# Kernel optimization log

Hardware: AMD Instinct MI355X
Metric: run time of the kernel (lower is better)

## Reference

```python
import jax, jax.numpy as jnp
import numpy as np

B, P, K = 32, 1024, 20  # clouds, points per cloud, kNN neighbors
EPS = 1e-5


def knn_idx(x, k):
    # x: [B,P,d] -> indices of k nearest neighbors (squared L2, includes self), [B,P,k]
    d2 = jnp.sum(x * x, axis=-1)
    dist = d2[:, :, None] + d2[:, None, :] - 2.0 * jnp.einsum('bpd,bqd->bpq', x, x)
    _, idx = jax.lax.top_k(-dist, k)
    return idx


def edge_conv(x, idx, msg_fn):
    # gather neighbor features, build [x_i, x_j - x_i] edge features, max-aggregate
    xj = jax.vmap(lambda xb, ib: xb[ib])(x, idx)            # [B,P,K,d]
    xi = jnp.broadcast_to(x[:, :, None, :], xj.shape)       # [B,P,K,d]
    e = jnp.concatenate([xi, xj - xi], axis=-1)             # [B,P,K,2d]
    return jnp.max(msg_fn(e), axis=2)                       # [B,P,out]


def setup_inputs() -> dict:
    key = jax.random.key(0)
    ks = jax.random.split(key, 5)
    s = 0.05
    return {
        'pos': jax.random.normal(ks[0], (B * P, 3), jnp.float32),
        'W1a': jax.random.normal(ks[1], (6, 64), jnp.float32) * s,
        'b1a': jnp.zeros((64,), jnp.float32),
        'g1': jnp.ones((64,), jnp.float32),
        'be1': jnp.zeros((64,), jnp.float32),
        'W1b': jax.random.normal(ks[2], (64, 64), jnp.float32) * s,
        'b1b': jnp.zeros((64,), jnp.float32),
        'W2': jax.random.normal(ks[3], (128, 128), jnp.float32) * s,
        'b2': jnp.zeros((128,), jnp.float32),
        'Wl': jax.random.normal(ks[4], (192, 128), jnp.float32) * s,
        'bl': jnp.zeros((128,), jnp.float32),
        'batch': jnp.repeat(jnp.arange(B, dtype=jnp.int32), P),
    }


def reference(pos, W1a, b1a, g1, be1, W1b, b1b, W2, b2, Wl, bl, batch):
    # batch is uniform-sized and sorted -> fixed reshape to [B,P,.]
    x0 = pos.reshape(B, P, 3)

    def mlp1(e):  # Linear(6,64) -> BatchNorm -> ReLU -> Linear(64,64)
        h = e @ W1a + b1a
        mu = jnp.mean(h, axis=(0, 1, 2))
        var = jnp.var(h, axis=(0, 1, 2))
        h = (h - mu) * jax.lax.rsqrt(var + EPS) * g1 + be1
        h = jax.nn.relu(h)
        return h @ W1b + b1b

    x1 = edge_conv(x0, knn_idx(x0, K), mlp1)                         # [B,P,64]
    x2 = edge_conv(x1, knn_idx(x1, K), lambda e: e @ W2 + b2)        # [B,P,128]
    h = jnp.concatenate([x1, x2], axis=-1) @ Wl + bl                 # [B,P,128]
    return jnp.max(h, axis=1)                                        # global_max_pool -> [B,128]
```

## Files before the change

### kernel.cpp

```cpp
#include <hip/hip_runtime.h>
#include <cfloat>
#include <cstdint>

#define NB 32
#define NP 1024
#define NK 20
#define NPTS 32768

typedef __attribute__((ext_vector_type(8))) short bf16x8;
typedef __attribute__((ext_vector_type(4))) float f32x4;

__device__ __forceinline__ unsigned bf16rne(float v) {
  const unsigned u = __float_as_uint(v);
  return (u + 0x7fffu + ((u >> 16) & 1u)) >> 16;
}

__device__ __forceinline__ float unsort_f(unsigned s) {
  const unsigned m = (~(unsigned)((int)s >> 31)) | 0x80000000u;
  return __uint_as_float(s ^ m);
}

__global__ __launch_bounds__(256) void kd2(const float* __restrict__ x, int dim,
                                           float* __restrict__ d2) {
  int p = blockIdx.x * 256 + threadIdx.x;
  if (p >= NPTS) return;
  if (dim == 64) {
    const float4* xr = (const float4*)(x + (size_t)p * 64);
    float s = 0.f;
#pragma unroll
    for (int dq = 0; dq < 16; dq++) {
      float4 v = xr[dq];
      s = fmaf(v.x, v.x, s);
      s = fmaf(v.y, v.y, s);
      s = fmaf(v.z, v.z, s);
      s = fmaf(v.w, v.w, s);
    }
    d2[p] = s;
  } else {
    float s = 0.f;
#pragma unroll
    for (int d = 0; d < 3; d++) {
      float v = x[p * 3 + d];
      s = fmaf(v, v, s);
    }
    d2[p] = s;
  }
}

__global__ __launch_bounds__(256) void kxprep(const float* __restrict__ x,
                                              unsigned short* __restrict__ Xh,
                                              unsigned short* __restrict__ Xl) {
  const int t = blockIdx.x * 256 + threadIdx.x;
  const int p = t >> 3, g = t & 7;
  const float4* xr = (const float4*)(x + (size_t)p * 64 + g * 8);
  const float4 v0 = xr[0];
  const float4 v1 = xr[1];
  const float vv[8] = {v0.x, v0.y, v0.z, v0.w, v1.x, v1.y, v1.z, v1.w};
  unsigned short h[8], l[8];
#pragma unroll
  for (int j = 0; j < 8; j++) {
    const float z = vv[j];
    const unsigned u = __float_as_uint(z);
    const unsigned hb = (u + 0x7fffu + ((u >> 16) & 1u)) & 0xffff0000u;
    h[j] = (unsigned short)(hb >> 16);
    l[j] = (unsigned short)bf16rne(z - __uint_as_float(hb));
  }
  const int off = (((p >> 4) * 2 + (g >> 2)) * 64 + ((g & 3) << 4) + (p & 15)) * 8;
  *(uint4*)&Xh[off] = *(const uint4*)&h[0];
  *(uint4*)&Xl[off] = *(const uint4*)&l[0];
}

__global__ __launch_bounds__(256) void kdistm(const unsigned short* __restrict__ Xh,
                                              const unsigned short* __restrict__ Xl,
                                              const float* __restrict__ d2,
                                              int c0, int nc, float* __restrict__ D) {
  const int lane = threadIdx.x & 63;
  const int w = threadIdx.x >> 6;
  const int cloud = blockIdx.x % nc;
  const int t = blockIdx.x / nc;
  const int tr0 = (t >> 3) * 128, tc0 = (t & 7) * 128;
  const int cb = (c0 + cloud) * 1024;
  const int rw = tr0 + w * 32;

  bf16x8 Ah[2][2], Al[2][2];
#pragma unroll
  for (int mt = 0; mt < 2; mt++)
#pragma unroll
    for (int ks = 0; ks < 2; ks++) {
      const int tg = (cb + rw + mt * 16) >> 4;
      const size_t base = ((size_t)(tg * 2 + ks) * 64 + lane) * 8;
      Ah[mt][ks] = *(const bf16x8*)&Xh[base];
      Al[mt][ks] = *(const bf16x8*)&Xl[base];
    }
  float d2r[2][4];
#pragma unroll
  for (int mt = 0; mt < 2; mt++)
#pragma unroll
    for (int r = 0; r < 4; r++)
      d2r[mt][r] = d2[cb + rw + mt * 16 + (lane >> 4) * 4 + r];

  for (int nt = 0; nt < 8; nt++) {
    const int cg = cb + tc0 + nt * 16;
    bf16x8 Bh2[2], Bl2[2];
#pragma unroll
    for (int ks = 0; ks < 2; ks++) {
      const int tg = cg >> 4;
      const size_t base = ((size_t)(tg * 2 + ks) * 64 + lane) * 8;
      Bh2[ks] = *(const bf16x8*)&Xh[base];
      Bl2[ks] = *(const bf16x8*)&Xl[base];
    }
    const float d2c = d2[cg + (lane & 15)];
#pragma unroll
    for (int mt = 0; mt < 2; mt++) {
      f32x4 C = {0.f, 0.f, 0.f, 0.f};
      C = __builtin_amdgcn_mfma_f32_16x16x32_bf16(Ah[mt][0], Bh2[0], C, 0, 0, 0);
      C = __builtin_amdgcn_mfma_f32_16x16x32_bf16(Ah[mt][0], Bl2[0], C, 0, 0, 0);
      C = __builtin_amdgcn_mfma_f32_16x16x32_bf16(Al[mt][0], Bh2[0], C, 0, 0, 0);
      C = __builtin_amdgcn_mfma_f32_16x16x32_bf16(Ah[mt][1], Bh2[1], C, 0, 0, 0);
      C = __builtin_amdgcn_mfma_f32_16x16x32_bf16(Ah[mt][1], Bl2[1], C, 0, 0, 0);
      C = __builtin_amdgcn_mfma_f32_16x16x32_bf16(Al[mt][1], Bh2[1], C, 0, 0, 0);
#pragma unroll
      for (int r = 0; r < 4; r++) {
        const int row = cloud * 1024 + rw + mt * 16 + (lane >> 4) * 4 + r;
        const int col = tc0 + nt * 16 + (lane & 15);
        D[(size_t)row * 1024 + col] = fmaf(-2.f, C[r], d2r[mt][r] + d2c);
      }
    }
  }
}

__device__ __forceinline__ void select20(const float* dv, unsigned long long* w,
                                         int lane, int pg, int gbase,
                                         int* __restrict__ idxo) {
  unsigned k32[16];
#pragma unroll
  for (int ii = 0; ii < 16; ii++) {
    unsigned u = __float_as_uint(dv[ii]);
    u ^= (((int)u >> 31) | 0x80000000u);
    k32[ii] = u;
  }
  unsigned lmn = k32[0];
#pragma unroll
  for (int ii = 1; ii < 16; ii++) lmn = k32[ii] < lmn ? k32[ii] : lmn;
  unsigned mn = lmn, mlm = lmn;
#pragma unroll
  for (int s = 1; s < 64; s <<= 1) {
    const unsigned a = __shfl_xor(mn, s, 64);
    const unsigned b = __shfl_xor(mlm, s, 64);
    mn = a < mn ? a : mn;
    mlm = b > mlm ? b : mlm;
  }
  unsigned lo32 = mn;
  unsigned long long hi32 = (unsigned long long)mlm + 1;
  float flo = unsort_f(mn), fhi = unsort_f(mlm);
  float clo = 0.f, chi = 140.f;
  unsigned m32 = 0;
  bool found = false;
  for (int it = 0; it < 40; ++it) {
    if (hi32 - (unsigned long long)lo32 <= 1) break;
    unsigned m;
    if (it < 6) {
      float fr = (42.f - clo) / (chi - clo);
      fr = fr < 0.04f ? 0.04f : (fr > 0.96f ? 0.96f : fr);
      const float pf = fmaf(fhi - flo, fr, flo);
      unsigned u = __float_as_uint(pf);
      u ^= (((int)u >> 31) | 0x80000000u);
      m = u;
      if (m <= lo32) m = lo32 + 1;
      if ((unsigned long long)m >= hi32) m = (unsigned)(hi32 - 1);
    } else {
      m = (unsigned)(lo32 + ((hi32 - lo32) >> 1));
    }
    int cnt = 0;
#pragma unroll
    for (int ii = 0; ii < 16; ii++) cnt += __popcll(__ballot(k32[ii] < m));
    if (cnt < 20) {
      lo32 = m;
      flo = unsort_f(m);
      clo = (float)cnt;
    } else if (cnt > 64) {
      hi32 = m;
      fhi = unsort_f(m);
      chi = (float)cnt;
    } else {
      m32 = m;
      found = true;
      break;
    }
  }

  if (found) {
    unsigned mask = 0;
#pragma unroll
    for (int ii = 0; ii < 16; ii++) mask |= (k32[ii] < m32) ? (1u << ii) : 0u;
    const int lc = __popc(mask);
    int x = lc;
#pragma unroll
    for (int s = 1; s < 64; s <<= 1) {
      const int y = __shfl_up(x, s, 64);
      if (lane >= s) x += y;
    }
    int off = x - lc;
    w[lane] = ~0ULL;
    __builtin_amdgcn_wave_barrier();
#pragma unroll
    for (int i = 0; i < 4; i++)
#pragma unroll
      for (int j = 0; j < 4; j++) {
        const int ii = i * 4 + j;
        if ((mask & (1u << ii)) && off < 64) {
          w[off] = ((unsigned long long)k32[ii] << 10) |
                   (unsigned)(i * 256 + (lane << 2) + j);
          off++;
        }
      }
    __builtin_amdgcn_wave_barrier();
    unsigned long long K = w[lane];
#pragma unroll
    for (int k = 2; k <= 64; k <<= 1) {
#pragma unroll
      for (int j2 = k >> 1; j2 > 0; j2 >>= 1) {
        const unsigned long long o = __shfl_xor(K, j2, 64);
        const bool takeMin = (((lane & j2) == 0) == ((lane & k) == 0));
        const bool lt = K < o;
        const unsigned long long sml = lt ? K : o;
        const unsigned long long big = lt ? o : K;
        K = takeMin ? sml : big;
      }
    }
    if (lane < NK) idxo[(size_t)pg * NK + lane] = gbase + (int)(K & 1023u);
  } else {
    unsigned long long lo64 = ((unsigned long long)lo32) << 10;
    unsigned long long hi64 = hi32 << 10;
    unsigned long long cut = hi64;
    for (int it = 0; it < 48 && (hi64 - lo64) > 1; ++it) {
      const unsigned long long m = lo64 + ((hi64 - lo64) >> 1);
      int cnt = 0;
#pragma unroll
      for (int ii = 0; ii < 16; ii++) {
        const unsigned long long key =
            ((unsigned long long)k32[ii] << 10) |
            (unsigned)(((ii >> 2) << 8) + (lane << 2) + (ii & 3));
        cnt += __popcll(__ballot(key < m));
      }
      if (cnt == 20) {
        cut = m;
        break;
      }
      if (cnt < 20)
        lo64 = m;
      else
        hi64 = m;
      cut = hi64;
    }
    int base = 0;
#pragma unroll
    for (int ii = 0; ii < 16; ii++) {
      const unsigned long long key =
          ((unsigned long long)k32[ii] << 10) |
          (unsigned)(((ii >> 2) << 8) + (lane << 2) + (ii & 3));
      const unsigned long long b = __ballot(key < cut);
      if (key < cut) {
        const int slot = base + __builtin_amdgcn_mbcnt_hi(
                                    (unsigned)(b >> 32),
                                    __builtin_amdgcn_mbcnt_lo((unsigned)b, 0));
        idxo[(size_t)pg * NK + slot] = gbase + (int)(key & 1023u);
      }
      base += __popcll(b);
    }
  }
}

__global__ __launch_bounds__(512) void kfsel1(const float* __restrict__ pos,
                                              const float* __restrict__ d2,
                                              int* __restrict__ idxo) {
  __shared__ float px[1024], py[1024], pz[1024], pd2[1024];
  __shared__ unsigned long long lw[8][64];
  const int tid = threadIdx.x;
  const int lane = tid & 63;
  const int w = tid >> 6;
  const int cloud = blockIdx.x >> 7;
  const int mb = blockIdx.x & 127;
  const int cb = cloud << 10;

  if (tid < 256) {
    const float4* ppos = (const float4*)(pos + (size_t)cb * 3 + tid * 12);
    const float4 a = ppos[0], b = ppos[1], c = ppos[2];
    *(float4*)&px[tid * 4] = make_float4(a.x, a.w, b.z, c.y);
    *(float4*)&py[tid * 4] = make_float4(a.y, b.x, b.w, c.z);
    *(float4*)&pz[tid * 4] = make_float4(a.z, b.y, c.x, c.w);
  }
  *(float2*)&pd2[tid * 2] = *(const float2*)(d2 + cb + tid * 2);
  __syncthreads();

  const int pl = mb * 8 + w;
  const float xi0 = px[pl], xi1 = py[pl], xi2 = pz[pl];
  const float dp = pd2[pl];
  float dv[16];
#pragma unroll
  for (int i = 0; i < 4; i++) {
    const float4 X = *(const float4*)&px[i * 256 + lane * 4];
    const float4 Y = *(const float4*)&py[i * 256 + lane * 4];
    const float4 Z = *(const float4*)&pz[i * 256 + lane * 4];
    const float4 Q = *(const float4*)&pd2[i * 256 + lane * 4];
    const float xs[4] = {X.x, X.y, X.z, X.w};
    const float ys[4] = {Y.x, Y.y, Y.z, Y.w};
    const float zs[4] = {Z.x, Z.y, Z.z, Z.w};
    const float qs[4] = {Q.x, Q.y, Q.z, Q.w};
#pragma unroll
    for (int j = 0; j < 4; j++) {
      float acc = 0.f;
      acc = fmaf(xi0, xs[j], acc);
      acc = fmaf(xi1, ys[j], acc);
      acc = fmaf(xi2, zs[j], acc);
      dv[i * 4 + j] = fmaf(-2.f, acc, dp + qs[j]);
    }
  }
  select20(dv, lw[w], lane, cb + pl, cb, idxo);
}

__global__ __launch_bounds__(256) void kselect2(const float* __restrict__ D,
                                                int c0, int* __restrict__ idxo) {
  __shared__ unsigned long long lw[4][64];
  const int lane = threadIdx.x & 63;
  const int sub = threadIdx.x >> 6;
  const int pchunk = blockIdx.x * 4 + sub;
  const int pg = c0 * 1024 + pchunk;
  const int gbase = (pg >> 10) << 10;

  float dv[16];
  const float4* dr = (const float4*)(D + (size_t)pchunk * 1024 + lane * 4);
#pragma unroll
  for (int i = 0; i < 4; i++) {
    const float4 d4 = dr[i * 64];
    dv[i * 4 + 0] = d4.x;
    dv[i * 4 + 1] = d4.y;
    dv[i * 4 + 2] = d4.z;
    dv[i * 4 + 3] = d4.w;
  }
  select20(dv, lw[sub], lane, pg, gbase, idxo);
}

__global__ __launch_bounds__(256) void kstats(const float* __restrict__ pos,
                                              const int* __restrict__ idx,
                                              double* __restrict__ Spart) {
  __shared__ float red[4][42];
  const int tid = threadIdx.x;
  const int w = tid >> 6;
  int p = blockIdx.x * 256 + tid;
  float xi0 = pos[p * 3], xi1 = pos[p * 3 + 1], xi2 = pos[p * 3 + 2];
  float s1[6];
  float s2[36];
#pragma unroll
  for (int a = 0; a < 6; a++) s1[a] = 0.f;
#pragma unroll
  for (int a = 0; a < 36; a++) s2[a] = 0.f;
  for (int k = 0; k < NK; k++) {
    int j = idx[p * NK + k];
    float e[6];
    e[0] = xi0;
    e[1] = xi1;
    e[2] = xi2;
    e[3] = pos[j * 3] - xi0;
    e[4] = pos[j * 3 + 1] - xi1;
    e[5] = pos[j * 3 + 2] - xi2;
#pragma unroll
    for (int a = 0; a < 6; a++) {
      s1[a] += e[a];
#pragma unroll
      for (int b = 0; b < 6; b++) s2[a * 6 + b] = fmaf(e[a], e[b], s2[a * 6 + b]);
    }
  }
#pragma unroll
  for (int a = 0; a < 6; a++) {
#pragma unroll
    for (int m = 1; m < 64; m <<= 1) s1[a] += __shfl_xor(s1[a], m, 64);
  }
#pragma unroll
  for (int a = 0; a < 36; a++) {
#pragma unroll
    for (int m = 1; m < 64; m <<= 1) s2[a] += __shfl_xor(s2[a], m, 64);
  }
  if ((tid & 63) == 0) {
#pragma unroll
    for (int a = 0; a < 6; a++) red[w][a] = s1[a];
#pragma unroll
    for (int a = 0; a < 36; a++) red[w][6 + a] = s2[a];
  }
  __syncthreads();
  if (tid < 42) {
    double t = (double)red[0][tid] + (double)red[1][tid] + (double)red[2][tid] +
               (double)red[3][tid];
    Spart[(size_t)blockIdx.x * 42 + tid] = t;
  }
}

__global__ void kbn(const double* __restrict__ Spart, const float* __restrict__ W1a,
                    const float* __restrict__ b1a, const float* __restrict__ g1,
                    const float* __restrict__ be1, const float* __restrict__ W1b,
                    float* __restrict__ ss, unsigned short* __restrict__ Bh,
                    unsigned short* __restrict__ Bl) {
  __shared__ double S[42];
  const int c = threadIdx.x;
  if (c < 42) {
    double t = 0.0;
    for (int b = 0; b < 128; b++) t += Spart[(size_t)b * 42 + c];
    S[c] = t;
  }
  for (int t = c; t < 4096; t += 256) {
    const int j = t & 7, L = (t >> 3) & 63, f = t >> 9;
    const int nt = f >> 1, ks = f & 1;
    const int k = ks * 32 + (L >> 4) * 8 + j;
    const int n = nt * 16 + (L & 15);
    const float wv = W1b[k * 64 + n];
    const unsigned u = __float_as_uint(wv);
    const unsigned hb = (u + 0x7fffu + ((u >> 16) & 1u)) & 0xffff0000u;
    Bh[t] = (unsigned short)(hb >> 16);
    Bl[t] = (unsigned short)bf16rne(wv - __uint_as_float(hb));
  }
  __syncthreads();
  if (c < 64) {
    double w[6];
#pragma unroll
    for (int d = 0; d < 6; d++) w[d] = (double)W1a[d * 64 + c];
    double b = (double)b1a[c];
    const double invN = 1.0 / (double)((size_t)NPTS * NK);
    double m1 = 0.0;
#pragma unroll
    for (int d = 0; d < 6; d++) m1 += w[d] * S[d];
    m1 *= invN;
    double q = 0.0;
#pragma unroll
    for (int a = 0; a < 6; a++)
#pragma unroll
      for (int d = 0; d < 6; d++) q += w[a] * w[d] * S[6 + a * 6 + d];
    q *= invN;
    double mu = m1 + b;
    double eh2 = q + 2.0 * b * m1 + b * b;
    double var = eh2 - mu * mu;
    if (var < 0.0) var = 0.0;
    double inv = 1.0 / sqrt(var + 1e-5);
    double sc = (double)g1[c] * inv;
    ss[c] = (float)sc;
    ss[64 + c] = (float)((double)be1[c] - mu * sc);
  }
}

#define EC1P 8
__global__ __launch_bounds__(256) void kec1(const float* __restrict__ pos,
                                            const int* __restrict__ idx,
                                            const float* __restrict__ ss,
                                            const float* __restrict__ W1a,
                                            const float* __restrict__ b1a,
                                            const unsigned short* __restrict__ Bh,
                                            const unsigned short* __restrict__ Bl,
                                            const float* __restrict__ b1b,
                                            float* __restrict__ x1) {
  __shared__ __align__(16) unsigned short Ah[4][3072];
  __shared__ __align__(16) unsigned short Al[4][3072];
  __shared__ float nbr[4][160];
  const int tid = threadIdx.x;
  const int lane = tid & 63;
  const int w = tid >> 6;
  const int p0 = blockIdx.x * EC1P + w * 2;

  unsigned short* ah = Ah[w];
  unsigned short* al = Al[w];
  float* nb = nbr[w];

  if (lane < 40) {
    const int j = idx[(size_t)p0 * NK + lane];
    nb[lane * 4 + 0] = pos[j * 3 + 0];
    nb[lane * 4 + 1] = pos[j * 3 + 1];
    nb[lane * 4 + 2] = pos[j * 3 + 2];
  }

  float wdf[3], wbt[3];
#pragma unroll
  for (int d = 0; d < 3; d++) {
    const float top = W1a[d * 64 + lane];
    const float bot = W1a[(3 + d) * 64 + lane];
    wdf[d] = top - bot;
    wbt[d] = bot;
  }
  const float b1 = b1a[lane];
  const float sc = ss[lane];
  const float sh = ss[64 + lane];
  const int lanehi = (((lane & 31) >> 3) * 128) + ((lane >> 5) * 512);
  const int lanelo = lane & 7;
  const int g3w = ((lane & 31) >> 3) + ((lane >> 5) << 2);
  __builtin_amdgcn_wave_barrier();

#pragma unroll
  for (int pp = 0; pp < 2; pp++) {
    const int p = p0 + pp;
    const float xi0 = pos[p * 3], xi1 = pos[p * 3 + 1], xi2 = pos[p * 3 + 2];
    const float pu = fmaf(xi2, wdf[2], fmaf(xi1, wdf[1], fmaf(xi0, wdf[0], b1)));
    for (int k = 0; k < NK; k++) {
      const int row = pp * NK + k;
      const float4 nbv = *(const float4*)&nb[row * 4];
      const float pv = fmaf(nbv.z, wbt[2], fmaf(nbv.y, wbt[1], nbv.x * wbt[0]));
      const float z = fmaxf(fmaf(pu + pv, sc, sh), 0.f);
      const unsigned u = __float_as_uint(z);
      const unsigned hb = (u + 0x7fffu + ((u >> 16) & 1u)) & 0xffff0000u;
      const int off =
          (row >> 4) * 1024 + lanehi + (((row & 15) ^ g3w) << 3) + lanelo;
      ah[off] = (unsigned short)(hb >> 16);
      al[off] = (unsigned short)bf16rne(z - __uint_as_float(hb));
    }
  }
  __builtin_amdgcn_wave_barrier();

  bf16x8 bh[4][2], bl[4][2];
#pragma unroll
  for (int nt = 0; nt < 4; nt++)
#pragma unroll
    for (int ks = 0; ks < 2; ks++) {
      const int base = ((nt * 2 + ks) * 64 + lane) * 8;
      bh[nt][ks] = *(const bf16x8*)&Bh[base];
      bl[nt][ks] = *(const bf16x8*)&Bl[base];
    }

  float pA[4], pB[4];
#pragma unroll
  for (int nt = 0; nt < 4; nt++) {
    pA[nt] = -FLT_MAX;
    pB[nt] = -FLT_MAX;
  }
  const int q4 = (lane >> 4) * 4;
  const int rb0 = (lane >> 4) * 128 + (((lane & 15) ^ (lane >> 4)) << 3);
  const int rb1 =
      512 + (lane >> 4) * 128 + (((lane & 15) ^ (4 + (lane >> 4))) << 3);

#pragma unroll
  for (int mt = 0; mt < 3; mt++) {
    const bf16x8 a_h0 = *(const bf16x8*)&ah[mt * 1024 + rb0];
    const bf16x8 a_l0 = *(const bf16x8*)&al[mt * 1024 + rb0];
    const bf16x8 a_h1 = *(const bf16x8*)&ah[mt * 1024 + rb1];
    const bf16x8 a_l1 = *(const bf16x8*)&al[mt * 1024 + rb1];
#pragma unroll
    for (int nt = 0; nt < 4; nt++) {
      f32x4 C = {0.f, 0.f, 0.f, 0.f};
      C = __builtin_amdgcn_mfma_f32_16x16x32_bf16(a_h0, bh[nt][0], C, 0, 0, 0);
      C = __builtin_amdgcn_mfma_f32_16x16x32_bf16(a_h0, bl[nt][0], C, 0, 0, 0);
      C = __builtin_amdgcn_mfma_f32_16x16x32_bf16(a_l0, bh[nt][0], C, 0, 0, 0);
      C = __builtin_amdgcn_mfma_f32_16x16x32_bf16(a_h1, bh[nt][1], C, 0, 0, 0);
      C = __builtin_amdgcn_mfma_f32_16x16x32_bf16(a_h1, bl[nt][1], C, 0, 0, 0);
      C = __builtin_amdgcn_mfma_f32_16x16x32_bf16(a_l1, bh[nt][1], C, 0, 0, 0);
#pragma unroll
      for (int r = 0; r < 4; r++) {
        const int row = mt * 16 + q4 + r;
        const float vv = C[r];
        if (row < NK) pA[nt] = fmaxf(pA[nt], vv);
        if (row >= NK && row < 2 * NK) pB[nt] = fmaxf(pB[nt], vv);
      }
    }
  }
#pragma unroll
  for (int s = 16; s < 64; s <<= 1) {
#pragma unroll
    for (int nt = 0; nt < 4; nt++) {
      pA[nt] = fmaxf(pA[nt], __shfl_xor(pA[nt], s, 64));
      pB[nt] = fmaxf(pB[nt], __shfl_xor(pB[nt], s, 64));
    }
  }
  if (lane < 16) {
#pragma unroll
    for (int nt = 0; nt < 4; nt++) {
      const float bb = b1b[nt * 16 + lane];
      x1[(size_t)p0 * 64 + nt * 16 + lane] = pA[nt] + bb;
      x1[(size_t)(p0 + 1) * 64 + nt * 16 + lane] = pB[nt] + bb;
    }
  }
}

__global__ __launch_bounds__(256) void kv(const float* __restrict__ x1,
                                          const float* __restrict__ W2,
                                          float* __restrict__ v) {
  const int c = threadIdx.x & 127;
  const int sub = threadIdx.x >> 7;
  float wv[64];
#pragma unroll
  for (int d = 0; d < 64; d++) wv[d] = W2[(64 + d) * 128 + c];
  const int pbase = blockIdx.x * 64 + sub * 32;
  for (int i = 0; i < 32; i++) {
    const int p = pbase + i;
    const float4* xr = (const float4*)(x1 + (size_t)p * 64);
    float a0 = 0.f, a1 = 0.f;
#pragma unroll
    for (int dq = 0; dq < 16; dq++) {
      float4 xv = xr[dq];
      a0 = fmaf(xv.x, wv[dq * 4 + 0], a0);
      a1 = fmaf(xv.y, wv[dq * 4 + 1], a1);
      a0 = fmaf(xv.z, wv[dq * 4 + 2], a0);
      a1 = fmaf(xv.w, wv[dq * 4 + 3], a1);
    }
    v[(size_t)p * 128 + c] = a0 + a1;
  }
}

__global__ __launch_bounds__(256) void kprep(const float* __restrict__ W2,
                                             const float* __restrict__ Wl,
                                             const float* __restrict__ b2,
                                             const float* __restrict__ bl,
                                             float* __restrict__ Bc,
                                             float* __restrict__ cb) {
  const int t = blockIdx.x * 256 + threadIdx.x;
  const int d = t >> 7, c = t & 127;
  float s = Wl[d * 128 + c];
  for (int e = 0; e < 128; e++)
    s = fmaf(W2[d * 128 + e] - W2[(64 + d) * 128 + e], Wl[(64 + e) * 128 + c], s);
  Bc[d * 128 + c] = s;
  Bc[(64 + 2 * d) * 128 + c] = Wl[(64 + 2 * d) * 128 + c];
  Bc[(64 + 2 * d + 1) * 128 + c] = Wl[(64 + 2 * d + 1) * 128 + c];
  if (d == 0) {
    float sb = bl[c];
    for (int e = 0; e < 128; e++) sb = fmaf(b2[e], Wl[(64 + e) * 128 + c], sb);
    cb[c] = sb;
  }
}

__global__ __launch_bounds__(256) void kprep2(const float* __restrict__ Bc,
                                              unsigned short* __restrict__ Bch,
                                              unsigned short* __restrict__ Bcl) {
  const int t = blockIdx.x * 256 + threadIdx.x;
  const int j = t & 7, L = (t >> 3) & 63, f = t >> 9;
  const int nt = f / 6, kc = f % 6;
  const int k = kc * 32 + ((L >> 4) << 3) + j;
  const int n = nt * 16 + (L & 15);
  const float wv = Bc[k * 128 + n];
  const unsigned u = __float_as_uint(wv);
  const unsigned hb = (u + 0x7fffu + ((u >> 16) & 1u)) & 0xffff0000u;
  Bch[t] = (unsigned short)(hb >> 16);
  Bcl[t] = (unsigned short)bf16rne(wv - __uint_as_float(hb));
}

__global__ __launch_bounds__(256) void kgemm(const float* __restrict__ x1,
                                             const float* __restrict__ v,
                                             const int* __restrict__ idx,
                                             const unsigned short* __restrict__ Bch,
                                             const unsigned short* __restrict__ Bcl,
                                             float* __restrict__ partial) {
  __shared__ int idxs[4][320];
  __shared__ __align__(16) float vlds[4][16][132];
  __shared__ float red[4][8][16];
  const int tid = threadIdx.x;
  const int lane = tid & 63;
  const int w = tid >> 6;
  const int cloud = blockIdx.x & 31;
  const int mb = blockIdx.x >> 5;
  const int pbase = cloud * 1024 + mb * 64;
  const int mrow = lane & 15, gsel = lane >> 4;
  const int m = w * 16 + mrow;

#pragma unroll
  for (int r = 0; r < 5; r++)
    idxs[w][r * 64 + lane] = idx[(size_t)(pbase + w * 16) * NK + r * 64 + lane];
  __builtin_amdgcn_wave_barrier();

  for (int pt = 0; pt < 16; pt++) {
    const int* ip = &idxs[w][pt * NK];
    float m0 = -FLT_MAX, m1 = -FLT_MAX;
#pragma unroll
    for (int k = 0; k < NK; k++) {
      const float2 val = *(const float2*)(v + (size_t)ip[k] * 128 + lane * 2);
      m0 = fmaxf(m0, val.x);
      m1 = fmaxf(m1, val.y);
    }
    *(float2*)&vlds[w][pt][lane * 2] = make_float2(m0, m1);
  }
  __builtin_amdgcn_wave_barrier();

  bf16x8 aH[6], aL[6];
#pragma unroll
  for (int kc = 0; kc < 2; kc++) {
    const float4* xr =
        (const float4*)(x1 + (size_t)(pbase + m) * 64 + kc * 32 + gsel * 8);
    const float4 v0 = xr[0], v1 = xr[1];
    const float vv[8] = {v0.x, v0.y, v0.z, v0.w, v1.x, v1.y, v1.z, v1.w};
    bf16x8 h, l;
#pragma unroll
    for (int j = 0; j < 8; j++) {
      const unsigned u = __float_as_uint(vv[j]);
      const unsigned hb = (u + 0x7fffu + ((u >> 16) & 1u)) & 0xffff0000u;
      h[j] = (short)(hb >> 16);
      l[j] = (short)bf16rne(vv[j] - __uint_as_float(hb));
    }
    aH[kc] = h;
    aL[kc] = l;
  }

#pragma unroll
  for (int g = 0; g < 4; g++) {
    const float* src = &vlds[w][mrow][g * 32 + gsel * 8];
    const float4 a = *(const float4*)(src);
    const float4 b = *(const float4*)(src + 4);
    const float vv[8] = {a.x, a.y, a.z, a.w, b.x, b.y, b.z, b.w};
    bf16x8 h, l;
#pragma unroll
    for (int j = 0; j < 8; j++) {
      const unsigned u = __float_as_uint(vv[j]);
      const unsigned hb = (u + 0x7fffu + ((u >> 16) & 1u)) & 0xffff0000u;
      h[j] = (short)(hb >> 16);
      l[j] = (short)bf16rne(vv[j] - __uint_as_float(hb));
    }
    aH[2 + g] = h;
    aL[2 + g] = l;
  }

  f32x4 acc[8];
#pragma unroll
  for (int nt = 0; nt < 8; nt++) acc[nt] = {0.f, 0.f, 0.f, 0.f};
#pragma unroll
  for (int nt = 0; nt < 8; nt++) {
#pragma unroll
    for (int kc = 0; kc < 6; kc++) {
      const size_t bo = ((size_t)(nt * 6 + kc) * 64 + lane) * 8;
      const bf16x8 b_h = *(const bf16x8*)&Bch[bo];
      const bf16x8 b_l = *(const bf16x8*)&Bcl[bo];
      acc[nt] = __builtin_amdgcn_mfma_f32_16x16x32_bf16(aH[kc], b_h, acc[nt], 0, 0, 0);
      acc[nt] = __builtin_amdgcn_mfma_f32_16x16x32_bf16(aH[kc], b_l, acc[nt], 0, 0, 0);
      acc[nt] = __builtin_amdgcn_mfma_f32_16x16x32_bf16(aL[kc], b_h, acc[nt], 0, 0, 0);
    }
  }

#pragma unroll
  for (int nt = 0; nt < 8; nt++) {
    float rm = fmaxf(fmaxf(acc[nt][0], acc[nt][1]), fmaxf(acc[nt][2], acc[nt][3]));
    rm = fmaxf(rm, __shfl_xor(rm, 16, 64));
    rm = fmaxf(rm, __shfl_xor(rm, 32, 64));
    if (lane < 16) red[w][nt][lane] = rm;
  }
  __syncthreads();
  if (tid < 128) {
    const int nt = tid >> 4, cc = tid & 15;
    const float m4 = fmaxf(fmaxf(red[0][nt][cc], red[1][nt][cc]),
                           fmaxf(red[2][nt][cc], red[3][nt][cc]));
    partial[(size_t)(cloud * 16 + mb) * 128 + tid] = m4;
  }
}

__global__ __launch_bounds__(256) void kred(const float* __restrict__ partial,
                                            const float* __restrict__ cb,
                                            float* __restrict__ out) {
  int t = blockIdx.x * 256 + threadIdx.x;
  int b = t >> 7, c = t & 127;
  float m = -FLT_MAX;
#pragma unroll
  for (int mb = 0; mb < 16; mb++) m = fmaxf(m, partial[(size_t)(b * 16 + mb) * 128 + c]);
  out[t] = m + cb[c];
}

extern "C" void kernel_launch(void* const* d_in, const int* in_sizes, int n_in,
                              void* d_out, int out_size, void* d_ws, size_t ws_size,
                              hipStream_t stream) {
  const float* pos = (const float*)d_in[0];
  const float* W1a = (const float*)d_in[1];
  const float* b1a = (const float*)d_in[2];
  const float* g1 = (const float*)d_in[3];
  const float* be1 = (const float*)d_in[4];
  const float* W1b = (const float*)d_in[5];
  const float* b1b = (const float*)d_in[6];
  const float* W2 = (const float*)d_in[7];
  const float* b2 = (const float*)d_in[8];
  const float* Wl = (const float*)d_in[9];
  const float* bl = (const float*)d_in[10];
  float* out = (float*)d_out;

  float* ws = (float*)d_ws;
  float* x1 = ws;
  float* v = ws + 2097152;
  int* idx = (int*)(ws + 6291456);
  float* d2b = ws + 6946816;
  double* Spart = (double*)(ws + 6979584);
  float* Bc = ws + 6990336;
  float* cb = ws + 7014912;
  float* ss = ws + 7015040;
  unsigned short* Bh = (unsigned short*)(ws + 7015168);
  unsigned short* Bl = (unsigned short*)(ws + 7017216);
  float* partial = ws + 7019264;
  unsigned short* Xfh = (unsigned short*)(ws + 7084800);
  unsigned short* Xfl = (unsigned short*)(ws + 8133376);
  unsigned short* Bch2 = (unsigned short*)(ws + 9181952);
  unsigned short* Bcl2 = (unsigned short*)(ws + 9194240);
  const size_t base = 9206528;
  float* D = ws + base;

  if (ws_size < (base + 1024 * 1024) * sizeof(float)) return;

  size_t avail = ws_size / sizeof(float) - base;
  int nc = 1;
  for (int c = 32; c >= 1; c >>= 1)
    if ((size_t)c * 1024 * 1024 <= avail) {
      nc = c;
      break;
    }

  kd2<<<128, 256, 0, stream>>>(pos, 3, d2b);
  kfsel1<<<NB * 128, 512, 0, stream>>>(pos, d2b, idx);

  kstats<<<128, 256, 0, stream>>>(pos, idx, Spart);
  kbn<<<1, 256, 0, stream>>>(Spart, W1a, b1a, g1, be1, W1b, ss, Bh, Bl);
  kec1<<<NPTS / EC1P, 256, 0, stream>>>(pos, idx, ss, W1a, b1a, Bh, Bl, b1b, x1);

  kd2<<<128, 256, 0, stream>>>(x1, 64, d2b);
  kxprep<<<1024, 256, 0, stream>>>(x1, Xfh, Xfl);
  for (int c0 = 0; c0 < NB; c0 += nc) {
    kdistm<<<nc * 64, 256, 0, stream>>>(Xfh, Xfl, d2b, c0, nc, D);
    kselect2<<<nc * 256, 256, 0, stream>>>(D, c0, idx);
  }

  kv<<<512, 256, 0, stream>>>(x1, W2, v);
  kprep<<<32, 256, 0, stream>>>(W2, Wl, b2, bl, Bc, cb);
  kprep2<<<96, 256, 0, stream>>>(Bc, Bch2, Bcl2);
  kgemm<<<512, 256, 0, stream>>>(x1, v, idx, Bch2, Bcl2, partial);
  kred<<<16, 256, 0, stream>>>(partial, cb, out);
}
```

Before: 324.6 us.

## Fuse second kNN distance matrix and top-k selection into one LDS-resident kernel

Replaces the two-kernel scheme, which wrote a full per-cloud 1024x1024 distance matrix to global memory and read it back for selection, with a single kernel. Each 512-thread block computes a 16-row strip of distances with MFMA into swizzled shared memory, then runs top-20 selection from LDS. This removes a large global write/read round trip and the chunked launch loop. In exchange each block recomputes reads of the column operands, with less reuse of the A tile than the old 128x128 tiles, and uses 64KB of LDS per block, which limits occupancy.

New measurement: 312.8 us. 1.04x faster.

```diff
diff --git a/kernel.cpp b/kernel.cpp
--- a/kernel.cpp
+++ b/kernel.cpp
@@ -68,65 +68,6 @@
   const int off = (((p >> 4) * 2 + (g >> 2)) * 64 + ((g & 3) << 4) + (p & 15)) * 8;
   *(uint4*)&Xh[off] = *(const uint4*)&h[0];
   *(uint4*)&Xl[off] = *(const uint4*)&l[0];
-}
-
-__global__ __launch_bounds__(256) void kdistm(const unsigned short* __restrict__ Xh,
-                                              const unsigned short* __restrict__ Xl,
-                                              const float* __restrict__ d2,
-                                              int c0, int nc, float* __restrict__ D) {
-  const int lane = threadIdx.x & 63;
-  const int w = threadIdx.x >> 6;
-  const int cloud = blockIdx.x % nc;
-  const int t = blockIdx.x / nc;
-  const int tr0 = (t >> 3) * 128, tc0 = (t & 7) * 128;
-  const int cb = (c0 + cloud) * 1024;
-  const int rw = tr0 + w * 32;
-
-  bf16x8 Ah[2][2], Al[2][2];
-#pragma unroll
-  for (int mt = 0; mt < 2; mt++)
-#pragma unroll
-    for (int ks = 0; ks < 2; ks++) {
-      const int tg = (cb + rw + mt * 16) >> 4;
-      const size_t base = ((size_t)(tg * 2 + ks) * 64 + lane) * 8;
-      Ah[mt][ks] = *(const bf16x8*)&Xh[base];
-      Al[mt][ks] = *(const bf16x8*)&Xl[base];
-    }
-  float d2r[2][4];
-#pragma unroll
-  for (int mt = 0; mt < 2; mt++)
-#pragma unroll
-    for (int r = 0; r < 4; r++)
-      d2r[mt][r] = d2[cb + rw + mt * 16 + (lane >> 4) * 4 + r];
-
-  for (int nt = 0; nt < 8; nt++) {
-    const int cg = cb + tc0 + nt * 16;
-    bf16x8 Bh2[2], Bl2[2];
-#pragma unroll
-    for (int ks = 0; ks < 2; ks++) {
-      const int tg = cg >> 4;
-      const size_t base = ((size_t)(tg * 2 + ks) * 64 + lane) * 8;
-      Bh2[ks] = *(const bf16x8*)&Xh[base];
-      Bl2[ks] = *(const bf16x8*)&Xl[base];
-    }
-    const float d2c = d2[cg + (lane & 15)];
-#pragma unroll
-    for (int mt = 0; mt < 2; mt++) {
-      f32x4 C = {0.f, 0.f, 0.f, 0.f};
-      C = __builtin_amdgcn_mfma_f32_16x16x32_bf16(Ah[mt][0], Bh2[0], C, 0, 0, 0);
-      C = __builtin_amdgcn_mfma_f32_16x16x32_bf16(Ah[mt][0], Bl2[0], C, 0, 0, 0);
-      C = __builtin_amdgcn_mfma_f32_16x16x32_bf16(Al[mt][0], Bh2[0], C, 0, 0, 0);
-      C = __builtin_amdgcn_mfma_f32_16x16x32_bf16(Ah[mt][1], Bh2[1], C, 0, 0, 0);
-      C = __builtin_amdgcn_mfma_f32_16x16x32_bf16(Ah[mt][1], Bl2[1], C, 0, 0, 0);
-      C = __builtin_amdgcn_mfma_f32_16x16x32_bf16(Al[mt][1], Bh2[1], C, 0, 0, 0);
-#pragma unroll
-      for (int r = 0; r < 4; r++) {
-        const int row = cloud * 1024 + rw + mt * 16 + (lane >> 4) * 4 + r;
-        const int col = tc0 + nt * 16 + (lane & 15);
-        D[(size_t)row * 1024 + col] = fmaf(-2.f, C[r], d2r[mt][r] + d2c);
-      }
-    }
-  }
 }
 
 __device__ __forceinline__ void select20(const float* dv, unsigned long long* w,
@@ -319,26 +260,74 @@
   select20(dv, lw[w], lane, cb + pl, cb, idxo);
 }
 
-__global__ __launch_bounds__(256) void kselect2(const float* __restrict__ D,
-                                                int c0, int* __restrict__ idxo) {
-  __shared__ unsigned long long lw[4][64];
+__global__ __launch_bounds__(512) void kdsel2(const unsigned short* __restrict__ Xh,
+                                              const unsigned short* __restrict__ Xl,
+                                              const float* __restrict__ d2,
+                                              int* __restrict__ idxo) {
+  __shared__ __align__(16) float Dl[16][1024];
+  __shared__ unsigned long long lw[8][64];
   const int lane = threadIdx.x & 63;
-  const int sub = threadIdx.x >> 6;
-  const int pchunk = blockIdx.x * 4 + sub;
-  const int pg = c0 * 1024 + pchunk;
-  const int gbase = (pg >> 10) << 10;
-
-  float dv[16];
-  const float4* dr = (const float4*)(D + (size_t)pchunk * 1024 + lane * 4);
-#pragma unroll
-  for (int i = 0; i < 4; i++) {
-    const float4 d4 = dr[i * 64];
-    dv[i * 4 + 0] = d4.x;
-    dv[i * 4 + 1] = d4.y;
-    dv[i * 4 + 2] = d4.z;
-    dv[i * 4 + 3] = d4.w;
-  }
-  select20(dv, lw[sub], lane, pg, gbase, idxo);
+  const int w = threadIdx.x >> 6;
+  const int cloud = blockIdx.x & 31;
+  const int rb = blockIdx.x >> 5;
+  const int cb = cloud * 1024;
+  const int rowb = rb * 16;
+
+  bf16x8 Ah[2], Al[2];
+#pragma unroll
+  for (int ks = 0; ks < 2; ks++) {
+    const int tg = (cb + rowb) >> 4;
+    const size_t base = ((size_t)(tg * 2 + ks) * 64 + lane) * 8;
+    Ah[ks] = *(const bf16x8*)&Xh[base];
+    Al[ks] = *(const bf16x8*)&Xl[base];
+  }
+  float d2r[4];
+#pragma unroll
+  for (int r = 0; r < 4; r++) d2r[r] = d2[cb + rowb + (lane >> 4) * 4 + r];
+
+#pragma unroll 2
+  for (int nt = 0; nt < 8; nt++) {
+    const int c0 = w * 128 + nt * 16;
+    const int cg = cb + c0;
+    bf16x8 Bh2[2], Bl2[2];
+#pragma unroll
+    for (int ks = 0; ks < 2; ks++) {
+      const int tg = cg >> 4;
+      const size_t base = ((size_t)(tg * 2 + ks) * 64 + lane) * 8;
+      Bh2[ks] = *(const bf16x8*)&Xh[base];
+      Bl2[ks] = *(const bf16x8*)&Xl[base];
+    }
+    const float d2c = d2[cg + (lane & 15)];
+    f32x4 C = {0.f, 0.f, 0.f, 0.f};
+    C = __builtin_amdgcn_mfma_f32_16x16x32_bf16(Ah[0], Bh2[0], C, 0, 0, 0);
+    C = __builtin_amdgcn_mfma_f32_16x16x32_bf16(Ah[0], Bl2[0], C, 0, 0, 0);
+    C = __builtin_amdgcn_mfma_f32_16x16x32_bf16(Al[0], Bh2[0], C, 0, 0, 0);
+    C = __builtin_amdgcn_mfma_f32_16x16x32_bf16(Ah[1], Bh2[1], C, 0, 0, 0);
+    C = __builtin_amdgcn_mfma_f32_16x16x32_bf16(Ah[1], Bl2[1], C, 0, 0, 0);
+    C = __builtin_amdgcn_mfma_f32_16x16x32_bf16(Al[1], Bh2[1], C, 0, 0, 0);
+#pragma unroll
+    for (int r = 0; r < 4; r++) {
+      const int row = (lane >> 4) * 4 + r;
+      const int col = c0 + (lane & 15);
+      Dl[row][col ^ ((row & 7) << 2)] = fmaf(-2.f, C[r], d2r[r] + d2c);
+    }
+  }
+  __syncthreads();
+
+  for (int pp = 0; pp < 2; pp++) {
+    const int pl = w * 2 + pp;
+    const int s = (pl & 7) << 2;
+    float dv[16];
+#pragma unroll
+    for (int i = 0; i < 4; i++) {
+      const float4 d4 = *(const float4*)&Dl[pl][(i * 256 + lane * 4) ^ s];
+      dv[i * 4 + 0] = d4.x;
+      dv[i * 4 + 1] = d4.y;
+      dv[i * 4 + 2] = d4.z;
+      dv[i * 4 + 3] = d4.w;
+    }
+    select20(dv, lw[w], lane, cb + rowb + pl, cb, idxo);
+  }
 }
 
 __global__ __launch_bounds__(256) void kstats(const float* __restrict__ pos,
@@ -784,17 +773,8 @@
   unsigned short* Bch2 = (unsigned short*)(ws + 9181952);
   unsigned short* Bcl2 = (unsigned short*)(ws + 9194240);
   const size_t base = 9206528;
-  float* D = ws + base;
-
-  if (ws_size < (base + 1024 * 1024) * sizeof(float)) return;
-
-  size_t avail = ws_size / sizeof(float) - base;
-  int nc = 1;
-  for (int c = 32; c >= 1; c >>= 1)
-    if ((size_t)c * 1024 * 1024 <= avail) {
-      nc = c;
-      break;
-    }
+
+  if (ws_size < base * sizeof(float)) return;
 
   kd2<<<128, 256, 0, stream>>>(pos, 3, d2b);
   kfsel1<<<NB * 128, 512, 0, stream>>>(pos, d2b, idx);
@@ -805,10 +785,7 @@
 
   kd2<<<128, 256, 0, stream>>>(x1, 64, d2b);
   kxprep<<<1024, 256, 0, stream>>>(x1, Xfh, Xfl);
-  for (int c0 = 0; c0 < NB; c0 += nc) {
-    kdistm<<<nc * 64, 256, 0, stream>>>(Xfh, Xfl, d2b, c0, nc, D);
-    kselect2<<<nc * 256, 256, 0, stream>>>(D, c0, idx);
-  }
+  kdsel2<<<NB * 64, 512, 0, stream>>>(Xfh, Xfl, d2b, idx);
 
   kv<<<512, 256, 0, stream>>>(x1, W2, v);
   kprep<<<32, 256, 0, stream>>>(W2, Wl, b2, bl, Bc, cb);
```
